# Optimization experiments

Hardware: AMD Instinct MI355X
Metric: run time of the kernel (lower is better)

The kernel has to match this reference:

```python
import jax, jax.numpy as jnp
import numpy as np

B, N, L = 32, 128, 1024
DRUG_DIM, TGT_DIM, HID, H = 256, 1280, 512, 8
HD = HID // H  # 64
NEG = jnp.float32(-1e9)


def setup_inputs() -> dict:
    key = jax.random.key(0)
    ks = jax.random.split(key, 9)
    drug_nodes = jax.random.normal(ks[0], (B, N, DRUG_DIM), dtype=jnp.float32)
    target_seq = jax.random.normal(ks[1], (B, L, TGT_DIM), dtype=jnp.float32)
    # masks: random valid lengths in [max//2, max], True = valid
    dlen = jax.random.randint(ks[2], (B,), N // 2, N + 1)
    tlen = jax.random.randint(ks[3], (B,), L // 2, L + 1)
    drug_mask = jnp.arange(N)[None, :] < dlen[:, None]
    target_mask = jnp.arange(L)[None, :] < tlen[:, None]
    # params (nn.Linear default init ~ U(-1/sqrt(fan_in), ...); randn*0.02 ok for a reference)
    Wd = jax.random.normal(ks[4], (DRUG_DIM, HID), dtype=jnp.float32) / np.sqrt(DRUG_DIM)
    bd = jnp.zeros((HID,), dtype=jnp.float32)
    Wt = jax.random.normal(ks[5], (TGT_DIM, HID), dtype=jnp.float32) / np.sqrt(TGT_DIM)
    bt = jnp.zeros((HID,), dtype=jnp.float32)
    Wb = jax.random.normal(ks[6], (H, HD, HD), dtype=jnp.float32) * 0.02
    return {"drug_nodes": drug_nodes, "drug_mask": drug_mask,
            "target_seq": target_seq, "target_mask": target_mask,
            "Wd": Wd, "bd": bd, "Wt": Wt, "bt": bt, "Wb": Wb}


def reference(drug_nodes, drug_mask, target_seq, target_mask, Wd, bd, Wt, bt, Wb):
    # project and split heads -> (h, B, n, hd) / (h, B, l, hd)
    d = drug_nodes @ Wd + bd                                  # (B, N, HID)
    t = target_seq @ Wt + bt                                  # (B, L, HID)
    dh = d.reshape(B, N, H, HD).transpose(2, 0, 1, 3)         # (H, B, N, HD)
    th = t.reshape(B, L, H, HD).transpose(2, 0, 1, 3)         # (H, B, L, HD)

    dW = jnp.einsum('hbnd,hde->hbne', dh, Wb)                 # bilinear map
    attn = jnp.einsum('hbne,hble->hbnl', dW, th)              # (H, B, N, L)

    mask = (drug_mask[:, :, None] & target_mask[:, None, :])[None]  # (1, B, N, L)
    scores = jnp.where(mask, attn, NEG)

    # drug-side softmax over protein residues (axis=-1), dropout is identity (eval)
    attn_d = jnp.where(mask, jax.nn.softmax(scores, axis=-1), 0.0)
    ctx_d = jnp.einsum('hbnl,hble->hbne', attn_d, th)         # (H, B, N, HD)
    dmf = drug_mask[None, :, :, None].astype(ctx_d.dtype)
    ctx_d = (ctx_d * dmf).sum(axis=2) / jnp.clip(dmf.sum(axis=2), 1.0)  # (H, B, HD)
    ctx_d = ctx_d.transpose(1, 0, 2).reshape(B, -1)           # (B, HID)

    # target-side softmax over atoms (axis=-2)
    attn_t = jnp.where(mask, jax.nn.softmax(scores, axis=-2), 0.0)
    ctx_t = jnp.einsum('hbnl,hbne->hble', attn_t, dh)         # (H, B, L, HD)
    tmf = target_mask[None, :, :, None].astype(ctx_t.dtype)
    ctx_t = (ctx_t * tmf).sum(axis=2) / jnp.clip(tmf.sum(axis=2), 1.0)  # (H, B, HD)
    ctx_t = ctx_t.transpose(1, 0, 2).reshape(B, -1)           # (B, HID)

    return jnp.concatenate([ctx_d, ctx_t], axis=-1)           # (B, 2*HID)
```

## Files before the change

### kernel.cpp

```cpp
#include <hip/hip_runtime.h>
#include <hip/hip_bf16.h>
#include <math.h>

#define B_ 32
#define N_ 128
#define L_ 1024
#define DD_ 256
#define TD_ 1280
#define HID_ 512
#define H_ 8
#define HD_ 64

#define WS_D    0
#define WS_RM   (WS_D   + 2097152)
#define WS_RIZ  (WS_RM  + 32768)
#define WS_RMT  (WS_RIZ + 32768)
#define WS_RZT  (WS_RMT + 524288)
#define WS_RWT  (WS_RZT + 524288)
#define WS_CNT  (WS_RWT + 524288)
#define WS_WT   (WS_CNT + 64)
#define WS_THB  (WS_WT  + 327680)
#define WS_DWB  (WS_THB + 8388608)

using bf16x8 = __attribute__((ext_vector_type(8))) short;
using u16x4 = __attribute__((ext_vector_type(4))) unsigned short;
using floatx4 = __attribute__((ext_vector_type(4))) float;

static __device__ __forceinline__ unsigned short f2bf(float f) {
  unsigned int u = __float_as_uint(f);
  unsigned int r = (u + 0x7FFFu + ((u >> 16) & 1u)) >> 16;
  return (unsigned short)r;
}
static __device__ __forceinline__ float bf2f(unsigned short s) {
  return __uint_as_float(((unsigned int)s) << 16);
}
static __device__ __forceinline__ void gload16(const void* g, void* l) {
  __builtin_amdgcn_global_load_lds(
      (const __attribute__((address_space(1))) void*)g,
      (__attribute__((address_space(3))) void*)l, 16, 0, 0);
}

__global__ __launch_bounds__(256) void count_kernel(const int* __restrict__ dmask,
                                                    const int* __restrict__ tmask,
                                                    int* __restrict__ cnts) {
  __shared__ int red[256];
  const int b = blockIdx.x, tid = threadIdx.x;
  const bool dint = (dmask[0] == 1);
  const bool tint = (tmask[0] == 1);
  int s = 0;
  if (dint) {
    for (int i = tid; i < N_; i += 256) s += (dmask[(size_t)b*N_ + i] != 0);
  } else {
    const unsigned char* p = (const unsigned char*)dmask;
    for (int i = tid; i < N_; i += 256) s += (p[(size_t)b*N_ + i] != 0);
  }
  red[tid] = s; __syncthreads();
  for (int off = 128; off > 0; off >>= 1) { if (tid < off) red[tid] += red[tid+off]; __syncthreads(); }
  if (tid == 0) cnts[b*2] = red[0];
  __syncthreads();
  s = 0;
  if (tint) {
    for (int i = tid; i < L_; i += 256) s += (tmask[(size_t)b*L_ + i] != 0);
  } else {
    const unsigned char* p = (const unsigned char*)tmask;
    for (int i = tid; i < L_; i += 256) s += (p[(size_t)b*L_ + i] != 0);
  }
  red[tid] = s; __syncthreads();
  for (int off = 128; off > 0; off >>= 1) { if (tid < off) red[tid] += red[tid+off]; __syncthreads(); }
  if (tid == 0) cnts[b*2+1] = red[0];
}

__global__ __launch_bounds__(256) void transpose_bf16_kernel(
    const float* __restrict__ W, unsigned short* __restrict__ WT, int K, int Nd) {
  __shared__ float tile[32][33];
  const int tid = threadIdx.x;
  const int n0 = blockIdx.x * 32, k0 = blockIdx.y * 32;
  const int c = tid & 31, r0 = tid >> 5;
#pragma unroll
  for (int i = 0; i < 4; i++) {
    const int r = r0 + i * 8;
    tile[c][r] = W[(size_t)(k0 + r) * Nd + n0 + c];
  }
  __syncthreads();
#pragma unroll
  for (int i = 0; i < 4; i++) {
    const int r = r0 + i * 8;
    WT[(size_t)(n0 + r) * K + k0 + c] = f2bf(tile[r][c]);
  }
}

__global__ __launch_bounds__(256, 2) void gemm_t_mfma_kernel(
    const float* __restrict__ A, const unsigned short* __restrict__ WT,
    const float* __restrict__ bias, unsigned short* __restrict__ thb, int K) {
  __shared__ __align__(16) unsigned short As[8192];
  __shared__ __align__(16) unsigned short Bs[16384];
  const int tid = threadIdx.x;
  const int lin = blockIdx.x;
  const int xcd = lin & 7, sq = lin >> 3;
  const int n_t = sq & 1, m_t = (sq >> 1) + xcd * 32;
  const int m0 = m_t * 128, n0 = n_t * 256;
  const int lane = tid & 63, wave = tid >> 6;
  const int wm = wave & 1, wn = wave >> 1;
  const int quad = lane >> 4, lrow = lane & 15;

  floatx4 acc[4][8];
#pragma unroll
  for (int i = 0; i < 4; i++)
#pragma unroll
    for (int j = 0; j < 8; j++) acc[i][j] = (floatx4){0.f, 0.f, 0.f, 0.f};

  int srcoffB[4][2];
#pragma unroll
  for (int call = 0; call < 4; call++) {
    const int i = call * 256 + tid;
    const int r = i >> 2;
    const int c = (i & 3) ^ ((r >> 1) & 3);
#pragma unroll
    for (int g = 0; g < 2; g++) srcoffB[call][g] = r * K + g * 32 + c * 8;
  }

  const int arow_ = wave * 4 + (lane >> 4);
  const int x_ = lane & 15;
  const int ag_ = x_ >> 3;
  const int acq_ = (x_ & 7) >> 1;
  const int ahalf_ = x_ & 1;

  const float* Abase = A + (size_t)m0 * K;
  const unsigned short* Bbase = WT + (size_t)n0 * K;

  float4 apf[8];

  auto aload = [&](int k0) {
#pragma unroll
    for (int i = 0; i < 8; i++)
      apf[i] = *(const float4*)(Abase + (size_t)(i * 16 + arow_) * K + k0 + x_ * 4);
  };
  auto awrite = [&]() {
#pragma unroll
    for (int i = 0; i < 8; i++) {
      const int r = i * 16 + arow_;
      const int sw = (r >> 1) & 3;
      u16x4 p;
      p[0] = f2bf(apf[i].x); p[1] = f2bf(apf[i].y);
      p[2] = f2bf(apf[i].z); p[3] = f2bf(apf[i].w);
      *(u16x4*)&As[ag_ * 4096 + (r * 4 + (acq_ ^ sw)) * 8 + ahalf_ * 4] = p;
    }
  };
  auto bstage = [&](int k0) {
#pragma unroll
    for (int g = 0; g < 2; g++)
#pragma unroll
      for (int call = 0; call < 4; call++) {
        const int dst = g * 8192 + (call * 256 + wave * 64) * 8;
        gload16(Bbase + k0 + srcoffB[call][g], &Bs[dst]);
      }
  };

  const int nkt = K / 64;
  aload(0);

  for (int t = 0; t < nkt; t++) {
    __syncthreads();
    bstage(t * 64);
    awrite();
    __syncthreads();
    if (t + 1 < nkt) aload((t + 1) * 64);
#pragma unroll
    for (int g = 0; g < 2; g++) {
      bf16x8 afr[4];
#pragma unroll
      for (int i = 0; i < 4; i++) {
        const int ar = wm * 64 + i * 16 + lrow;
        afr[i] = *(const bf16x8*)&As[g * 4096 + (ar * 4 + (quad ^ ((ar >> 1) & 3))) * 8];
      }
#pragma unroll
      for (int jh = 0; jh < 2; jh++) {
        bf16x8 bfr[4];
#pragma unroll
        for (int j = 0; j < 4; j++) {
          const int br = wn * 128 + (jh * 4 + j) * 16 + lrow;
          bfr[j] = *(const bf16x8*)&Bs[g * 8192 + (br * 4 + (quad ^ ((br >> 1) & 3))) * 8];
        }
#pragma unroll
        for (int i = 0; i < 4; i++)
#pragma unroll
          for (int j = 0; j < 4; j++)
            acc[i][jh * 4 + j] = __builtin_amdgcn_mfma_f32_16x16x32_bf16(
                afr[i], bfr[j], acc[i][jh * 4 + j], 0, 0, 0);
      }
    }
  }

  float bj[8];
#pragma unroll
  for (int j = 0; j < 8; j++) bj[j] = bias[n0 + wn * 128 + j * 16 + lrow];
#pragma unroll
  for (int i = 0; i < 4; i++) {
#pragma unroll
    for (int j = 0; j < 8; j++) {
      const int gcol = n0 + wn * 128 + j * 16 + lrow;
      const int hh = gcol >> 6, e = gcol & 63;
#pragma unroll
      for (int r = 0; r < 4; r++) {
        const int grow = m0 + wm * 64 + i * 16 + quad * 4 + r;
        const int bb = grow >> 10, l = grow & 1023;
        thb[(((size_t)bb * H_ + hh) * L_ + l) * HD_ + e] = f2bf(acc[i][j][r] + bj[j]);
      }
    }
  }
}

__global__ __launch_bounds__(256) void gemm_bias_kernel(
    const float* __restrict__ A, const float* __restrict__ W,
    const float* __restrict__ bias, float* __restrict__ C,
    int M, int K, int Nd) {
  __shared__ float As[8][132];
  __shared__ float Bs[8][132];
  const int tid = threadIdx.x;
  const int m0 = blockIdx.y * 128, n0 = blockIdx.x * 128;
  const int lr = tid >> 1, lc = (tid & 1) * 4;
  const int wr = tid >> 5, wc = (tid & 31) * 4;
  const int tm = (tid >> 4) * 4, tn = (tid & 15) * 4;

  float acc[2][2][4][4];
#pragma unroll
  for (int a = 0; a < 2; a++)
#pragma unroll
    for (int bq = 0; bq < 2; bq++)
#pragma unroll
      for (int i = 0; i < 4; i++)
#pragma unroll
        for (int j = 0; j < 4; j++) acc[a][bq][i][j] = 0.f;

  const float* Aptr = A + (size_t)(m0 + lr) * K + lc;
  const float* Wptr = W + (size_t)wr * Nd + n0 + wc;

  for (int k0 = 0; k0 < K; k0 += 8) {
    float4 a4 = *(const float4*)(Aptr + k0);
    float4 w4 = *(const float4*)(Wptr + (size_t)k0 * Nd);
    __syncthreads();
    As[lc+0][lr] = a4.x; As[lc+1][lr] = a4.y; As[lc+2][lr] = a4.z; As[lc+3][lr] = a4.w;
    *(float4*)&Bs[wr][wc] = w4;
    __syncthreads();
#pragma unroll
    for (int kk = 0; kk < 8; kk++) {
      float4 a0 = *(const float4*)&As[kk][tm];
      float4 a1 = *(const float4*)&As[kk][tm + 64];
      float4 b0 = *(const float4*)&Bs[kk][tn];
      float4 b1 = *(const float4*)&Bs[kk][tn + 64];
      const float av0[4] = {a0.x, a0.y, a0.z, a0.w};
      const float av1[4] = {a1.x, a1.y, a1.z, a1.w};
      const float bv0[4] = {b0.x, b0.y, b0.z, b0.w};
      const float bv1[4] = {b1.x, b1.y, b1.z, b1.w};
#pragma unroll
      for (int i = 0; i < 4; i++)
#pragma unroll
        for (int j = 0; j < 4; j++) {
          acc[0][0][i][j] += av0[i] * bv0[j];
          acc[0][1][i][j] += av0[i] * bv1[j];
          acc[1][0][i][j] += av1[i] * bv0[j];
          acc[1][1][i][j] += av1[i] * bv1[j];
        }
    }
  }
  float4 bias0 = *(const float4*)&bias[n0 + tn];
  float4 bias1 = *(const float4*)&bias[n0 + tn + 64];
  const float bb0[4] = {bias0.x, bias0.y, bias0.z, bias0.w};
  const float bb1[4] = {bias1.x, bias1.y, bias1.z, bias1.w};
#pragma unroll
  for (int mh = 0; mh < 2; mh++)
#pragma unroll
    for (int i = 0; i < 4; i++) {
      const int row = m0 + mh * 64 + tm + i;
      float* cp = C + (size_t)row * Nd + n0;
      float4 o0, o1;
      o0.x = acc[mh][0][i][0] + bb0[0]; o0.y = acc[mh][0][i][1] + bb0[1];
      o0.z = acc[mh][0][i][2] + bb0[2]; o0.w = acc[mh][0][i][3] + bb0[3];
      o1.x = acc[mh][1][i][0] + bb1[0]; o1.y = acc[mh][1][i][1] + bb1[1];
      o1.z = acc[mh][1][i][2] + bb1[2]; o1.w = acc[mh][1][i][3] + bb1[3];
      *(float4*)(cp + tn) = o0;
      *(float4*)(cp + tn + 64) = o1;
    }
}

__global__ __launch_bounds__(256) void dw_kernel(
    const float* __restrict__ dproj, const float* __restrict__ Wb,
    unsigned short* __restrict__ dWb) {
  __shared__ float wb_s[64 * 64];
  const int tid = threadIdx.x;
  const int hb = blockIdx.x, b = hb >> 3, h = hb & 7;
  for (int i = tid; i < 4096; i += 256) wb_s[i] = Wb[(size_t)h * 4096 + i];
  __syncthreads();
  const int n = tid >> 1, half = tid & 1;
  float acc[32];
#pragma unroll
  for (int e = 0; e < 32; e++) acc[e] = 0.f;
  const float* dpr = dproj + ((size_t)(b * N_ + n)) * HID_ + h * HD_;
  for (int k = 0; k < 64; k++) {
    const float a = dpr[k];
    const float* wr = &wb_s[k * 64 + half * 32];
#pragma unroll
    for (int e = 0; e < 32; e++) acc[e] += a * wr[e];
  }
  unsigned short* outp = dWb + ((size_t)hb * N_ + n) * HD_ + half * 32;
#pragma unroll
  for (int e = 0; e < 32; e++) outp[e] = f2bf(acc[e]);
}

__device__ __forceinline__ void mfma_S_tile(
    const unsigned short* __restrict__ thp, const unsigned short* __restrict__ dwp,
    float* __restrict__ S_s, int ncnt, int lv, int tid) {
  const int lane = tid & 63, wave = tid >> 6;
  const int quad = lane >> 4, lr = lane & 15;
  const int noff = (wave & 1) * 64, loff = (wave >> 1) * 32;

  floatx4 acc[4][2];
#pragma unroll
  for (int i = 0; i < 4; i++)
#pragma unroll
    for (int j = 0; j < 2; j++) acc[i][j] = (floatx4){0.f, 0.f, 0.f, 0.f};

#pragma unroll
  for (int kc = 0; kc < 2; kc++) {
    bf16x8 bfr[2];
#pragma unroll
    for (int j = 0; j < 2; j++)
      bfr[j] = *(const bf16x8*)&thp[(size_t)(loff + j * 16 + lr) * HD_ + kc * 32 + quad * 8];
#pragma unroll
    for (int i = 0; i < 4; i++) {
      bf16x8 afr = *(const bf16x8*)&dwp[(size_t)(noff + i * 16 + lr) * HD_ + kc * 32 + quad * 8];
#pragma unroll
      for (int j = 0; j < 2; j++)
        acc[i][j] = __builtin_amdgcn_mfma_f32_16x16x32_bf16(afr, bfr[j], acc[i][j], 0, 0, 0);
    }
  }
#pragma unroll
  for (int i = 0; i < 4; i++)
#pragma unroll
    for (int j = 0; j < 2; j++)
#pragma unroll
      for (int r = 0; r < 4; r++) {
        const int n = noff + i * 16 + quad * 4 + r;
        const int li = loff + j * 16 + lr;
        const bool ok = (n < ncnt) && (li < lv);
        S_s[n * 69 + li] = ok ? acc[i][j][r] : -1e9f;
      }
}

__global__ __launch_bounds__(256, 4) void attn_stats_kernel(
    const unsigned short* __restrict__ thb, const unsigned short* __restrict__ dWb,
    const int* __restrict__ cnts, float* __restrict__ rwt,
    float* __restrict__ rmt, float* __restrict__ rzt) {
  __shared__ float S_s[128 * 69];
  __shared__ float red[256];
  __shared__ float zb_s[256], wb_s[256];
  __shared__ float cm_s[64], ics_s[64];
  const int tid = threadIdx.x;
  const int hb = blockIdx.x >> 4, lt = blockIdx.x & 15;
  const int b = hb >> 3;
  const int ncnt = cnts[b * 2], lcnt = cnts[b * 2 + 1];
  const int l0g = lt * 64;
  if (l0g >= lcnt) return;
  const int lv = min(64, lcnt - l0g);

  mfma_S_tile(thb + ((size_t)hb * L_ + l0g) * HD_, dWb + (size_t)hb * N_ * HD_,
              S_s, ncnt, lv, tid);
  __syncthreads();

  {
    const int l = tid & 63, q = tid >> 6;
    float pm = -INFINITY;
    for (int n = q * 32; n < q * 32 + 32; n++) pm = fmaxf(pm, S_s[n * 69 + l]);
    red[tid] = pm;
  }
  __syncthreads();
  if (tid < 64)
    cm_s[tid] = fmaxf(fmaxf(red[tid], red[tid + 64]), fmaxf(red[tid + 128], red[tid + 192]));
  __syncthreads();
  {
    const int l = tid & 63, q = tid >> 6;
    const float cm = cm_s[l];
    float ps = 0.f;
    for (int n = q * 32; n < q * 32 + 32; n++) ps += __expf(S_s[n * 69 + l] - cm);
    red[tid] = ps;
  }
  __syncthreads();
  if (tid < 64)
    ics_s[tid] = 1.f / (red[tid] + red[tid + 64] + red[tid + 128] + red[tid + 192]);
  __syncthreads();
  {
    const int n = tid & 127, half = tid >> 7;
    const float* Sr = &S_s[n * 69];
    const int lb = half * 32, le = min(lb + 32, lv);
    float tmax = -INFINITY;
    for (int l = lb; l < le; l++) tmax = fmaxf(tmax, Sr[l]);
    red[tid] = tmax;
    __syncthreads();
    const float tm = fmaxf(red[n], red[n + 128]);
    float z = 0.f, w = 0.f;
    for (int l = lb; l < le; l++) {
      const float s = Sr[l];
      z += __expf(s - tm);
      w += __expf(s - cm_s[l]) * ics_s[l];
    }
    zb_s[tid] = z; wb_s[tid] = w;
    __syncthreads();
    if (tid < 128) {
      const size_t o = ((size_t)hb * 16 + lt) * 128 + tid;
      rmt[o] = tm;
      rzt[o] = zb_s[tid] + zb_s[tid + 128];
      rwt[o] = wb_s[tid] + wb_s[tid + 128];
    }
  }
}

__global__ __launch_bounds__(256) void attn_combine_kernel(
    const float* __restrict__ rmt, const float* __restrict__ rzt,
    const float* __restrict__ rwt, const float* __restrict__ dproj,
    const int* __restrict__ cnts, float* __restrict__ rm_g,
    float* __restrict__ riz_g, float* __restrict__ outp) {
  __shared__ float red[256];
  __shared__ float w_s[128];
  const int tid = threadIdx.x;
  const int hb = blockIdx.x, b = hb >> 3, h = hb & 7;
  const int ncnt = cnts[b * 2], lcnt = cnts[b * 2 + 1];
  const int ntl = (lcnt + 63) >> 6;
  if (tid < 128) {
    const int n = tid;
    float m = -INFINITY;
    for (int t = 0; t < ntl; t++)
      m = fmaxf(m, rmt[((size_t)hb * 16 + t) * 128 + n]);
    float Z = 0.f, w = 0.f;
    for (int t = 0; t < ntl; t++) {
      const size_t o = ((size_t)hb * 16 + t) * 128 + n;
      Z += rzt[o] * __expf(rmt[o] - m);
      w += rwt[o];
    }
    rm_g[hb * 128 + n] = m;
    riz_g[hb * 128 + n] = (n < ncnt) ? 1.f / Z : 0.f;
    w_s[n] = (n < ncnt) ? w : 0.f;
  }
  __syncthreads();
  const int e = tid & 63, q = tid >> 6;
  float p = 0.f;
  const int nb = q * 32, ne = min(nb + 32, ncnt);
  for (int n = nb; n < ne; n++)
    p += w_s[n] * dproj[((size_t)(b * N_ + n)) * HID_ + h * HD_ + e];
  red[tid] = p;
  __syncthreads();
  if (tid < 64) {
    const float s = red[tid] + red[tid + 64] + red[tid + 128] + red[tid + 192];
    outp[(size_t)b * (2 * HID_) + HID_ + h * HD_ + tid] = s / (float)lcnt;
  }
}

__global__ __launch_bounds__(256, 4) void attn_v_kernel(
    const unsigned short* __restrict__ thb, const unsigned short* __restrict__ dWb,
    const int* __restrict__ cnts, const float* __restrict__ rm_g,
    const float* __restrict__ riz_g, float* __restrict__ outp) {
  __shared__ float S_s[128 * 69];
  __shared__ float red[256];
  __shared__ float rm_s[128], riz_s[128], v_s[64];
  const int tid = threadIdx.x;
  const int hb = blockIdx.x >> 4, lt = blockIdx.x & 15;
  const int b = hb >> 3, h = hb & 7;
  const int ncnt = cnts[b * 2], lcnt = cnts[b * 2 + 1];
  const int l0g = lt * 64;
  if (l0g >= lcnt) return;
  const int lv = min(64, lcnt - l0g);

  if (tid < 128) {
    rm_s[tid] = rm_g[hb * 128 + tid];
    riz_s[tid] = riz_g[hb * 128 + tid];
  }
  const unsigned short* thp = thb + ((size_t)hb * L_ + l0g) * HD_;
  mfma_S_tile(thp, dWb + (size_t)hb * N_ * HD_, S_s, ncnt, lv, tid);
  __syncthreads();

  {
    const int l = tid & 63, q = tid >> 6;
    float vp = 0.f;
    for (int n = q * 32; n < q * 32 + 32; n++)
      vp += __expf(S_s[n * 69 + l] - rm_s[n]) * riz_s[n];
    red[tid] = vp;
  }
  __syncthreads();
  const float incnt = 1.f / (float)ncnt;
  if (tid < 64) {
    const float v = (tid < lv)
        ? (red[tid] + red[tid + 64] + red[tid + 128] + red[tid + 192]) * incnt
        : 0.f;
    v_s[tid] = v;
  }
  __syncthreads();
  {
    const int e = tid & 63, q = tid >> 6;
    float p = 0.f;
    for (int l = q * 16; l < q * 16 + 16; l++)
      p += v_s[l] * bf2f(thp[(size_t)l * HD_ + e]);
    red[tid] = p;
  }
  __syncthreads();
  if (tid < 64) {
    const float s = red[tid] + red[tid + 64] + red[tid + 128] + red[tid + 192];
    if (s != 0.f)
      atomicAdd(&outp[(size_t)b * (2 * HID_) + h * HD_ + tid], s);
  }
}

extern "C" void kernel_launch(void* const* d_in, const int* in_sizes, int n_in,
                              void* d_out, int out_size, void* d_ws, size_t ws_size,
                              hipStream_t stream) {
  const float* drug = (const float*)d_in[0];
  const int* dmask = (const int*)d_in[1];
  const float* tseq = (const float*)d_in[2];
  const int* tmask = (const int*)d_in[3];
  const float* Wd = (const float*)d_in[4];
  const float* bd = (const float*)d_in[5];
  const float* Wt = (const float*)d_in[6];
  const float* bt = (const float*)d_in[7];
  const float* Wb = (const float*)d_in[8];
  float* out = (float*)d_out;
  float* ws = (float*)d_ws;

  float* dp = ws + WS_D;
  float* rm = ws + WS_RM;
  float* riz = ws + WS_RIZ;
  float* rmt = ws + WS_RMT;
  float* rzt = ws + WS_RZT;
  float* rwt = ws + WS_RWT;
  int* cnts = (int*)(ws + WS_CNT);
  unsigned short* wtT = (unsigned short*)(ws + WS_WT);
  unsigned short* thb = (unsigned short*)(ws + WS_THB);
  unsigned short* dWb = (unsigned short*)(ws + WS_DWB);

  count_kernel<<<B_, 256, 0, stream>>>(dmask, tmask, cnts);
  hipMemsetAsync(out, 0, (size_t)out_size * sizeof(float), stream);
  transpose_bf16_kernel<<<dim3(HID_ / 32, TD_ / 32), 256, 0, stream>>>(Wt, wtT, TD_, HID_);
  gemm_t_mfma_kernel<<<(HID_ / 256) * ((B_ * L_) / 128), 256, 0, stream>>>(
      tseq, wtT, bt, thb, TD_);
  gemm_bias_kernel<<<dim3(HID_ / 128, (B_ * N_) / 128), 256, 0, stream>>>(
      drug, Wd, bd, dp, B_ * N_, DD_, HID_);
  dw_kernel<<<B_ * H_, 256, 0, stream>>>(dp, Wb, dWb);
  attn_stats_kernel<<<B_ * H_ * 16, 256, 0, stream>>>(thb, dWb, cnts, rwt, rmt, rzt);
  attn_combine_kernel<<<B_ * H_, 256, 0, stream>>>(rmt, rzt, rwt, dp, cnts, rm, riz, out);
  attn_v_kernel<<<B_ * H_ * 16, 256, 0, stream>>>(thb, dWb, cnts, rm, riz, out);
}
```

Before: 430.3 us.

## Double-buffer GEMM B tiles, stage dW inputs in LDS, skip masked rows in softmax loops

The target-projection GEMM now keeps two LDS buffers for the B tile, so loads for the next k-tile are issued before the MFMA work on the current one. The dW kernel stages the drug projection rows in shared memory and reads Wb with float4 loads. The column-softmax and context loops now stop at the valid drug or target count instead of iterating over padded rows. Double buffering doubles the B shared-memory footprint (about 80KB per block with As), which may prevent the two blocks per CU requested by launch_bounds. Skipping padded rows assumes the masked S entries need not be read, which matches the later masking of those rows.

```diff
diff --git a/kernel.cpp b/kernel.cpp
--- a/kernel.cpp
+++ b/kernel.cpp
@@ -93,7 +93,7 @@
     const float* __restrict__ A, const unsigned short* __restrict__ WT,
     const float* __restrict__ bias, unsigned short* __restrict__ thb, int K) {
   __shared__ __align__(16) unsigned short As[8192];
-  __shared__ __align__(16) unsigned short Bs[16384];
+  __shared__ __align__(16) unsigned short Bs[2][16384];
   const int tid = threadIdx.x;
   const int lin = blockIdx.x;
   const int xcd = lin & 7, sq = lin >> 3;
@@ -146,25 +146,30 @@
       *(u16x4*)&As[ag_ * 4096 + (r * 4 + (acq_ ^ sw)) * 8 + ahalf_ * 4] = p;
     }
   };
-  auto bstage = [&](int k0) {
+  auto bstage = [&](int buf, int k0) {
 #pragma unroll
     for (int g = 0; g < 2; g++)
 #pragma unroll
       for (int call = 0; call < 4; call++) {
         const int dst = g * 8192 + (call * 256 + wave * 64) * 8;
-        gload16(Bbase + k0 + srcoffB[call][g], &Bs[dst]);
+        gload16(Bbase + k0 + srcoffB[call][g], &Bs[buf][dst]);
       }
   };
 
   const int nkt = K / 64;
+
   aload(0);
-
+  bstage(0, 0);
+  awrite();
+  __syncthreads();
+
+  int cur = 0;
   for (int t = 0; t < nkt; t++) {
-    __syncthreads();
-    bstage(t * 64);
-    awrite();
-    __syncthreads();
-    if (t + 1 < nkt) aload((t + 1) * 64);
+    const int nxt = cur ^ 1;
+    if (t + 1 < nkt) {
+      aload((t + 1) * 64);
+      bstage(nxt, (t + 1) * 64);
+    }
 #pragma unroll
     for (int g = 0; g < 2; g++) {
       bf16x8 afr[4];
@@ -179,7 +184,7 @@
 #pragma unroll
         for (int j = 0; j < 4; j++) {
           const int br = wn * 128 + (jh * 4 + j) * 16 + lrow;
-          bfr[j] = *(const bf16x8*)&Bs[g * 8192 + (br * 4 + (quad ^ ((br >> 1) & 3))) * 8];
+          bfr[j] = *(const bf16x8*)&Bs[cur][g * 8192 + (br * 4 + (quad ^ ((br >> 1) & 3))) * 8];
         }
 #pragma unroll
         for (int i = 0; i < 4; i++)
@@ -189,6 +194,12 @@
                 afr[i], bfr[j], acc[i][jh * 4 + j], 0, 0, 0);
       }
     }
+    __syncthreads();
+    if (t + 1 < nkt) {
+      awrite();
+    }
+    __syncthreads();
+    cur = nxt;
   }
 
   float bj[8];
@@ -287,20 +298,32 @@
     const float* __restrict__ dproj, const float* __restrict__ Wb,
     unsigned short* __restrict__ dWb) {
   __shared__ float wb_s[64 * 64];
+  __shared__ float dp_s[128 * 64];
   const int tid = threadIdx.x;
   const int hb = blockIdx.x, b = hb >> 3, h = hb & 7;
   for (int i = tid; i < 4096; i += 256) wb_s[i] = Wb[(size_t)h * 4096 + i];
+#pragma unroll
+  for (int rep = 0; rep < 8; rep++) {
+    const int idx = rep * 256 + tid;
+    const int row = idx >> 4, c4 = (idx & 15) * 4;
+    *(float4*)&dp_s[row * 64 + c4] =
+        *(const float4*)&dproj[((size_t)(b * N_ + row)) * HID_ + h * HD_ + c4];
+  }
   __syncthreads();
   const int n = tid >> 1, half = tid & 1;
   float acc[32];
 #pragma unroll
   for (int e = 0; e < 32; e++) acc[e] = 0.f;
-  const float* dpr = dproj + ((size_t)(b * N_ + n)) * HID_ + h * HD_;
+  const float* dpr = &dp_s[n * 64];
   for (int k = 0; k < 64; k++) {
     const float a = dpr[k];
     const float* wr = &wb_s[k * 64 + half * 32];
 #pragma unroll
-    for (int e = 0; e < 32; e++) acc[e] += a * wr[e];
+    for (int e4 = 0; e4 < 8; e4++) {
+      float4 w = *(const float4*)&wr[e4 * 4];
+      acc[e4*4+0] += a * w.x; acc[e4*4+1] += a * w.y;
+      acc[e4*4+2] += a * w.z; acc[e4*4+3] += a * w.w;
+    }
   }
   unsigned short* outp = dWb + ((size_t)hb * N_ + n) * HD_ + half * 32;
 #pragma unroll
@@ -369,8 +392,9 @@
 
   {
     const int l = tid & 63, q = tid >> 6;
+    const int ne = min(q * 32 + 32, ncnt);
     float pm = -INFINITY;
-    for (int n = q * 32; n < q * 32 + 32; n++) pm = fmaxf(pm, S_s[n * 69 + l]);
+    for (int n = q * 32; n < ne; n++) pm = fmaxf(pm, S_s[n * 69 + l]);
     red[tid] = pm;
   }
   __syncthreads();
@@ -379,9 +403,10 @@
   __syncthreads();
   {
     const int l = tid & 63, q = tid >> 6;
+    const int ne = min(q * 32 + 32, ncnt);
     const float cm = cm_s[l];
     float ps = 0.f;
-    for (int n = q * 32; n < q * 32 + 32; n++) ps += __expf(S_s[n * 69 + l] - cm);
+    for (int n = q * 32; n < ne; n++) ps += __expf(S_s[n * 69 + l] - cm);
     red[tid] = ps;
   }
   __syncthreads();
@@ -479,8 +504,9 @@
 
   {
     const int l = tid & 63, q = tid >> 6;
+    const int ne = min(q * 32 + 32, ncnt);
     float vp = 0.f;
-    for (int n = q * 32; n < q * 32 + 32; n++)
+    for (int n = q * 32; n < ne; n++)
       vp += __expf(S_s[n * 69 + l] - rm_s[n]) * riz_s[n];
     red[tid] = vp;
   }
@@ -495,8 +521,9 @@
   __syncthreads();
   {
     const int e = tid & 63, q = tid >> 6;
+    const int le = min(q * 16 + 16, lv);
     float p = 0.f;
-    for (int l = q * 16; l < q * 16 + 16; l++)
+    for (int l = q * 16; l < le; l++)
       p += v_s[l] * bf2f(thp[(size_t)l * HD_ + e]);
     red[tid] = p;
   }
```

Result: slower. 463.1 us (+7.6%).
